# Performance work log

Hardware: AMD Instinct MI355X
Metric: run time of the kernel (lower is better)

## Reference

```python
import jax, jax.numpy as jnp
import numpy as np
from jax import lax

EPS = 1e-05


def rmsnorm_axis1(x, w, eps=EPS):
    # RMS over channel axis (axis=1), scale by per-channel weight
    ms = jnp.mean(x * x, axis=1, keepdims=True)
    return x * lax.rsqrt(ms + eps) * w[None, :, None]


def dwconv1d(x, w, b, dilation):
    # x: [B, C, L]; w: [C, 1, K] depthwise (feature_group_count=C)
    pad = (w.shape[-1] - 1) // 2 * dilation
    y = lax.conv_general_dilated(
        x, w, window_strides=(1,), padding=[(pad, pad)],
        rhs_dilation=(dilation,), dimension_numbers=('NCH', 'OIH', 'NCH'),
        feature_group_count=x.shape[1])
    return y + b[None, :, None]


def setup_inputs() -> dict:
    key = jax.random.key(0)
    ks = jax.random.split(key, 12)
    B, C, L, K = 16, 512, 2048, 3
    s = 1.0 / np.sqrt(C)
    return {
        'number_log': jax.random.normal(ks[0], (B,), jnp.float32),
        'x': jax.random.normal(ks[1], (B, C, L), jnp.float32),
        'pre_w': jnp.ones((C,), jnp.float32),
        'conv_w': jax.random.normal(ks[2], (C, 1, K), jnp.float32) * 0.3,
        'conv_b': jnp.zeros((C,), jnp.float32),
        'conv1_w': jax.random.normal(ks[3], (C, 1, K), jnp.float32) * 0.3,
        'conv1_b': jnp.zeros((C,), jnp.float32),
        'conv2_w': jax.random.normal(ks[4], (C, 1, K), jnp.float32) * 0.3,
        'conv2_b': jnp.zeros((C,), jnp.float32),
        'gate_w': jax.random.normal(ks[5], (C, C), jnp.float32) * s,
        'gate_b': jnp.zeros((C,), jnp.float32),
        'post_w': jnp.ones((C,), jnp.float32),
        'logits_w': jax.random.normal(ks[6], (1, C, 1), jnp.float32) * s,
    }


def reference(number_log, x, pre_w, conv_w, conv_b, conv1_w, conv1_b,
              conv2_w, conv2_b, gate_w, gate_b, post_w, logits_w):
    # pre_norm over channel axis
    x_norm = rmsnorm_axis1(x, pre_w)
    # three dilated depthwise conv branches, summed
    x_d = (dwconv1d(x_norm, conv_w, conv_b, 1)
           + dwconv1d(x_norm, conv1_w, conv1_b, 2)
           + dwconv1d(x_norm, conv2_w, conv2_b, 4))
    # gate: Linear over channel dim of transposed input, SiLU
    gate = jax.nn.silu(jnp.einsum('bcl,dc->bdl', x_norm, gate_w)
                       + gate_b[None, :, None])
    x_d = rmsnorm_axis1(x_d * gate, post_w)
    # logits: 1x1 conv C->1, no bias
    out = jnp.einsum('bcl,oc->bol', x + x_d, logits_w[:, :, 0])
    return out
```

## Files before the change

### kernel.cpp

```cpp
#include <hip/hip_runtime.h>
#include <hip/hip_bf16.h>

#define BB 16
#define CC 512
#define LL 2048

typedef float f32x4 __attribute__((ext_vector_type(4)));
typedef short s16x8 __attribute__((ext_vector_type(8)));

static __device__ __forceinline__ float bf2f(unsigned short u) {
    union { unsigned int i; float f; } v; v.i = ((unsigned int)u) << 16; return v.f;
}
static __device__ __forceinline__ unsigned short f2bf(float f) {
    union { float fv; unsigned int i; } v; v.fv = f;
    unsigned int x = v.i;
    return (unsigned short)((x + 0x7FFFu + ((x >> 16) & 1u)) >> 16);
}

__global__ void k0_cast(const float* __restrict__ gw, unsigned short* __restrict__ gwb) {
    int i = blockIdx.x * 256 + threadIdx.x;
    if (i < CC * CC) gwb[i] = f2bf(gw[i]);
}

#define K1_ST 520
__global__ __launch_bounds__(256) void k1_rms_t(
    const float* __restrict__ x, const float* __restrict__ pre_w,
    unsigned short* __restrict__ xnt, float* __restrict__ invr) {
    __shared__ unsigned short tile[32 * K1_ST];
    __shared__ float red[32 * 33];
    __shared__ float pwS[CC];
    __shared__ float ivS[32];
    const int tid = threadIdx.x;
    const int b  = blockIdx.x >> 6;
    const int lt = blockIdx.x & 63;
    const int l0 = lt * 32;
    const float* xb = x + (size_t)(b * CC) * LL + l0;

    for (int i = tid; i < CC; i += 256) pwS[i] = pre_w[i];

    const int lq = tid & 7;
    const int cr = tid >> 3;
    f32x4 ssq = {0.f, 0.f, 0.f, 0.f};
    #pragma unroll
    for (int p = 0; p < 16; ++p) {
        int c = p * 32 + cr;
        f32x4 v = *(const f32x4*)(xb + (size_t)c * LL + lq * 4);
        #pragma unroll
        for (int r = 0; r < 4; ++r) {
            ssq[r] += v[r] * v[r];
            tile[(lq * 4 + r) * K1_ST + c] = f2bf(v[r]);
        }
    }
    #pragma unroll
    for (int r = 0; r < 4; ++r) red[(lq * 4 + r) * 33 + cr] = ssq[r];
    __syncthreads();
    if (tid < 32) {
        float s = 0.f;
        #pragma unroll
        for (int g = 0; g < 32; ++g) s += red[tid * 33 + g];
        float iv = rsqrtf(s * (1.0f / CC) + 1e-5f);
        ivS[tid] = iv;
        invr[b * LL + l0 + tid] = iv;
    }
    __syncthreads();
    unsigned short* xo = xnt + ((size_t)b * LL + l0) * CC;
    #pragma unroll
    for (int p = 0; p < 8; ++p) {
        int g = p * 256 + tid;
        int l = g >> 6, c8 = (g & 63) * 8;
        s16x8 t = *(const s16x8*)&tile[l * K1_ST + c8];
        f32x4 w0 = *(const f32x4*)&pwS[c8];
        f32x4 w1 = *(const f32x4*)&pwS[c8 + 4];
        float iv = ivS[l];
        s16x8 o;
        #pragma unroll
        for (int r = 0; r < 4; ++r) {
            o[r]     = (short)f2bf(bf2f((unsigned short)t[r])     * iv * w0[r]);
            o[r + 4] = (short)f2bf(bf2f((unsigned short)t[r + 4]) * iv * w1[r]);
        }
        *(s16x8*)(xo + (size_t)l * CC + c8) = o;
    }
}

__global__ __launch_bounds__(512, 4) void k2_gemm(
    const unsigned short* __restrict__ gwb,
    const unsigned short* __restrict__ xnt,
    const float* __restrict__ gate_b,
    unsigned short* __restrict__ gate) {
    __shared__ unsigned short As[3][128 * 32];
    __shared__ unsigned short Bs[3][256 * 32];
    const int tid = threadIdx.x;
    const int w = tid >> 6, lane = tid & 63;
    const int lo = lane & 15, hi = lane >> 4;
    const int wm = w >> 2, wn = w & 3;
    const int nt = blockIdx.x, mt = blockIdx.y, b = blockIdx.z;
    const int m0 = mt * 128, n0 = nt * 256;
    const unsigned short* Ab = gwb;
    const unsigned short* Bb = xnt + (size_t)b * LL * CC;

    #define STG(kt_, buf_)                                                            \
        {                                                                             \
            {                                                                         \
                int row_ = tid >> 2, gin_ = tid & 3;                                  \
                int ks_ = (kt_) * 32 + ((gin_ ^ ((row_ >> 1) & 3)) * 8);              \
                __builtin_amdgcn_global_load_lds(                                     \
                    (const __attribute__((address_space(1))) void*)(Ab + (size_t)(m0 + row_) * CC + ks_), \
                    (__attribute__((address_space(3))) void*)(&As[buf_][tid * 8]),    \
                    16, 0, 0);                                                        \
            }                                                                         \
            _Pragma("unroll")                                                         \
            for (int s_ = 0; s_ < 2; ++s_) {                                          \
                int g_ = tid + s_ * 512;                                              \
                int row_ = g_ >> 2, gin_ = g_ & 3;                                    \
                int ks_ = (kt_) * 32 + ((gin_ ^ ((row_ >> 1) & 3)) * 8);              \
                __builtin_amdgcn_global_load_lds(                                     \
                    (const __attribute__((address_space(1))) void*)(Bb + (size_t)(n0 + row_) * CC + ks_), \
                    (__attribute__((address_space(3))) void*)(&Bs[buf_][g_ * 8]),     \
                    16, 0, 0);                                                        \
            }                                                                         \
        }

    f32x4 acc[4][4] = {};
    const int fsw = (lo >> 1) & 3;

    STG(0, 0);
    STG(1, 1);
    #pragma unroll
    for (int kt = 0; kt < 16; ++kt) {
        const int buf = kt % 3;
        if (kt < 14) {
            STG(kt + 2, (kt + 2) % 3);
            asm volatile("s_waitcnt vmcnt(6)" ::: "memory");
        } else if (kt == 14) {
            asm volatile("s_waitcnt vmcnt(3)" ::: "memory");
        } else {
            asm volatile("s_waitcnt vmcnt(0)" ::: "memory");
        }
        __builtin_amdgcn_s_barrier();
        s16x8 af[4], bfr[4];
        #pragma unroll
        for (int mi = 0; mi < 4; ++mi)
            af[mi] = *(const s16x8*)&As[buf][(wm * 64 + mi * 16 + lo) * 32 + ((hi ^ fsw) * 8)];
        #pragma unroll
        for (int ni = 0; ni < 4; ++ni)
            bfr[ni] = *(const s16x8*)&Bs[buf][(wn * 64 + ni * 16 + lo) * 32 + ((hi ^ fsw) * 8)];
        __builtin_amdgcn_s_setprio(1);
        #pragma unroll
        for (int mi = 0; mi < 4; ++mi)
            #pragma unroll
            for (int ni = 0; ni < 4; ++ni)
                acc[mi][ni] = __builtin_amdgcn_mfma_f32_16x16x32_bf16(
                    af[mi], bfr[ni], acc[mi][ni], 0, 0, 0);
        __builtin_amdgcn_s_setprio(0);
        asm volatile("" ::: "memory");
        __builtin_amdgcn_s_barrier();
    }
    #undef STG

    #pragma unroll
    for (int mi = 0; mi < 4; ++mi) {
        #pragma unroll
        for (int ni = 0; ni < 4; ++ni) {
            int n = n0 + wn * 64 + ni * 16 + lo;
            int d0 = m0 + wm * 64 + mi * 16 + hi * 4;
            #pragma unroll
            for (int r = 0; r < 4; ++r) {
                int d = d0 + r;
                float z = acc[mi][ni][r] + gate_b[d];
                float s = z / (1.0f + __expf(-z));
                gate[((size_t)(b * CC + d)) * LL + n] = f2bf(s);
            }
        }
    }
}

__global__ __launch_bounds__(256) void k3a(
    const float* __restrict__ x, const float* __restrict__ invr,
    const unsigned short* __restrict__ gate,
    const float* __restrict__ cw0, const float* __restrict__ cb0,
    const float* __restrict__ cw1, const float* __restrict__ cb1,
    const float* __restrict__ cw2, const float* __restrict__ cb2,
    const float* __restrict__ pre_w, const float* __restrict__ post_w,
    const float* __restrict__ lw, float* __restrict__ part) {
    __shared__ float tapS[64][8];
    __shared__ float biasS[64], preS[64], lwS[64], pwlwS[64];
    __shared__ float ivs[136];
    __shared__ float red[8][128][3];
    const int tid = threadIdx.x;
    const int lt = blockIdx.x;
    const int cc = blockIdx.y;
    const int b  = blockIdx.z;
    const int l0 = lt * 128;
    const int c0 = cc * 64;

    if (tid < 64) {
        int c = c0 + tid;
        float w10 = cw0[c*3], w11 = cw0[c*3+1], w12 = cw0[c*3+2];
        float w20 = cw1[c*3], w21 = cw1[c*3+1], w22 = cw1[c*3+2];
        float w40 = cw2[c*3], w41 = cw2[c*3+1], w42 = cw2[c*3+2];
        tapS[tid][0] = w40; tapS[tid][1] = w20; tapS[tid][2] = w10;
        tapS[tid][3] = w11 + w21 + w41;
        tapS[tid][4] = w12; tapS[tid][5] = w22; tapS[tid][6] = w42;
        biasS[tid] = cb0[c] + cb1[c] + cb2[c];
        preS[tid]  = pre_w[c];
        float lwc = lw[c];
        lwS[tid] = lwc;
        pwlwS[tid] = post_w[c] * lwc;
    }
    if (tid < 136) {
        int lg = l0 - 4 + tid;
        ivs[tid] = (lg >= 0 && lg < LL) ? invr[b * LL + lg] : 0.f;
    }
    __syncthreads();

    const int li = tid & 31, ci = tid >> 5;
    const int lq = l0 + li * 4;
    float iv[12];
    #pragma unroll
    for (int j = 0; j < 12; ++j) iv[j] = ivs[li * 4 + j];

    const int ia = (lq - 4 < 0) ? 0 : lq - 4;
    const int ic = (lq + 4 > LL - 4) ? LL - 4 : lq + 4;

    float ass[4] = {}, adp[4] = {}, adx[4] = {};
    const float* xbase = x + ((size_t)(b * CC + c0)) * LL;
    const unsigned short* gbase = gate + ((size_t)(b * CC + c0)) * LL;

    #pragma unroll
    for (int j = 0; j < 8; ++j) {
        const int cl = ci * 8 + j;
        const float* xr = xbase + (size_t)cl * LL;
        f32x4 xa = *(const f32x4*)(xr + ia);
        f32x4 xm = *(const f32x4*)(xr + lq);
        f32x4 xc = *(const f32x4*)(xr + ic);
        uint2 gu = *(const uint2*)(gbase + (size_t)cl * LL + lq);
        float g[4];
        g[0] = bf2f((unsigned short)(gu.x & 0xffff));
        g[1] = bf2f((unsigned short)(gu.x >> 16));
        g[2] = bf2f((unsigned short)(gu.y & 0xffff));
        g[3] = bf2f((unsigned short)(gu.y >> 16));
        float z[12];
        #pragma unroll
        for (int r = 0; r < 4; ++r) {
            z[r]     = xa[r] * iv[r];
            z[r + 4] = xm[r] * iv[r + 4];
            z[r + 8] = xc[r] * iv[r + 8];
        }
        const float t0 = tapS[cl][0], t1 = tapS[cl][1], t2 = tapS[cl][2],
                    t3 = tapS[cl][3], t4 = tapS[cl][4], t5 = tapS[cl][5],
                    t6 = tapS[cl][6];
        const float pre = preS[cl], bias = biasS[cl], pwlw = pwlwS[cl], lwc = lwS[cl];
        #pragma unroll
        for (int k = 0; k < 4; ++k) {
            float s = t0 * z[k] + t1 * z[k + 2] + t2 * z[k + 3] + t3 * z[k + 4]
                    + t4 * z[k + 5] + t5 * z[k + 6] + t6 * z[k + 8];
            float p = (pre * s + bias) * g[k];
            ass[k] += p * p;
            adp[k] += p * pwlw;
            adx[k] += xm[k] * lwc;
        }
    }
    #pragma unroll
    for (int k = 0; k < 4; ++k) {
        red[ci][li * 4 + k][0] = ass[k];
        red[ci][li * 4 + k][1] = adp[k];
        red[ci][li * 4 + k][2] = adx[k];
    }
    __syncthreads();
    if (tid < 128) {
        float s0 = 0.f, s1 = 0.f, s2 = 0.f;
        #pragma unroll
        for (int g2 = 0; g2 < 8; ++g2) {
            s0 += red[g2][tid][0];
            s1 += red[g2][tid][1];
            s2 += red[g2][tid][2];
        }
        float* pp = part + (((size_t)(b * 8 + cc)) * LL + l0 + tid) * 3;
        pp[0] = s0; pp[1] = s1; pp[2] = s2;
    }
}

__global__ __launch_bounds__(256) void k3b(
    const float* __restrict__ part, float* __restrict__ out) {
    int gl = blockIdx.x * 256 + threadIdx.x;
    int b = gl >> 11, l = gl & 2047;
    float s0 = 0.f, s1 = 0.f, s2 = 0.f;
    #pragma unroll
    for (int cc2 = 0; cc2 < 8; ++cc2) {
        const float* pp = part + (((size_t)(b * 8 + cc2)) * LL + l) * 3;
        s0 += pp[0]; s1 += pp[1]; s2 += pp[2];
    }
    out[gl] = s2 + rsqrtf(s0 * (1.0f / CC) + 1e-5f) * s1;
}

extern "C" void kernel_launch(void* const* d_in, const int* in_sizes, int n_in,
                              void* d_out, int out_size, void* d_ws, size_t ws_size,
                              hipStream_t stream) {
    const float* x      = (const float*)d_in[1];
    const float* pre_w  = (const float*)d_in[2];
    const float* cw0    = (const float*)d_in[3];
    const float* cb0    = (const float*)d_in[4];
    const float* cw1    = (const float*)d_in[5];
    const float* cb1    = (const float*)d_in[6];
    const float* cw2    = (const float*)d_in[7];
    const float* cb2    = (const float*)d_in[8];
    const float* gw     = (const float*)d_in[9];
    const float* gb     = (const float*)d_in[10];
    const float* post_w = (const float*)d_in[11];
    const float* lw     = (const float*)d_in[12];
    float* out = (float*)d_out;

    char* ws = (char*)d_ws;
    unsigned short* gwb  = (unsigned short*)(ws);
    unsigned short* xnt  = (unsigned short*)(ws + 524288);
    float*          invr = (float*)(ws + 524288 + 33554432);
    unsigned short* gate = (unsigned short*)(ws + 524288 + 33554432 + 131072);
    float*          part = (float*)(ws + 524288);

    hipLaunchKernelGGL(k0_cast,  dim3((CC * CC + 255) / 256), dim3(256), 0, stream, gw, gwb);
    hipLaunchKernelGGL(k1_rms_t, dim3(BB * (LL / 32)),        dim3(256), 0, stream, x, pre_w, xnt, invr);
    hipLaunchKernelGGL(k2_gemm,  dim3(LL / 256, CC / 128, BB), dim3(512), 0, stream, gwb, xnt, gb, gate);
    hipLaunchKernelGGL(k3a,      dim3(LL / 128, CC / 64, BB), dim3(256), 0, stream,
                       x, invr, gate, cw0, cb0, cw1, cb1, cw2, cb2, pre_w, post_w, lw, part);
    hipLaunchKernelGGL(k3b,      dim3(BB * LL / 256),         dim3(256), 0, stream, part, out);
}
```

Baseline: 78.60 us.

## Drop LDS staging in gate GEMM, load MFMA fragments directly from global

The gate GEMM no longer stages A and B tiles through a triple-buffered LDS pipeline with barriers. Each wave instead loads its MFMA fragments straight from global memory (relying on L1/L2) and computes a 64x64 tile, with blocks shrunk to 256 threads and a 64-row M tile. This removes the barrier and LDS traffic overhead but loses cross-wave reuse, since the A tile is loaded by all four waves. It also drops explicit prefetching, which exposes global-load latency per k-step.

```diff
diff --git a/kernel.cpp b/kernel.cpp
--- a/kernel.cpp
+++ b/kernel.cpp
@@ -82,87 +82,45 @@
     }
 }
 
-__global__ __launch_bounds__(512, 4) void k2_gemm(
+__global__ __launch_bounds__(256, 3) void k2_gemm(
     const unsigned short* __restrict__ gwb,
     const unsigned short* __restrict__ xnt,
     const float* __restrict__ gate_b,
     unsigned short* __restrict__ gate) {
-    __shared__ unsigned short As[3][128 * 32];
-    __shared__ unsigned short Bs[3][256 * 32];
     const int tid = threadIdx.x;
     const int w = tid >> 6, lane = tid & 63;
     const int lo = lane & 15, hi = lane >> 4;
-    const int wm = w >> 2, wn = w & 3;
     const int nt = blockIdx.x, mt = blockIdx.y, b = blockIdx.z;
-    const int m0 = mt * 128, n0 = nt * 256;
-    const unsigned short* Ab = gwb;
-    const unsigned short* Bb = xnt + (size_t)b * LL * CC;
-
-    #define STG(kt_, buf_)                                                            \
-        {                                                                             \
-            {                                                                         \
-                int row_ = tid >> 2, gin_ = tid & 3;                                  \
-                int ks_ = (kt_) * 32 + ((gin_ ^ ((row_ >> 1) & 3)) * 8);              \
-                __builtin_amdgcn_global_load_lds(                                     \
-                    (const __attribute__((address_space(1))) void*)(Ab + (size_t)(m0 + row_) * CC + ks_), \
-                    (__attribute__((address_space(3))) void*)(&As[buf_][tid * 8]),    \
-                    16, 0, 0);                                                        \
-            }                                                                         \
-            _Pragma("unroll")                                                         \
-            for (int s_ = 0; s_ < 2; ++s_) {                                          \
-                int g_ = tid + s_ * 512;                                              \
-                int row_ = g_ >> 2, gin_ = g_ & 3;                                    \
-                int ks_ = (kt_) * 32 + ((gin_ ^ ((row_ >> 1) & 3)) * 8);              \
-                __builtin_amdgcn_global_load_lds(                                     \
-                    (const __attribute__((address_space(1))) void*)(Bb + (size_t)(n0 + row_) * CC + ks_), \
-                    (__attribute__((address_space(3))) void*)(&Bs[buf_][g_ * 8]),     \
-                    16, 0, 0);                                                        \
-            }                                                                         \
-        }
+    const int m0 = mt * 64;
+    const int n0 = nt * 256 + w * 64;
+
+    const unsigned short* Ap = gwb + (size_t)(m0 + lo) * CC + hi * 8;
+    const unsigned short* Bp = xnt + (size_t)b * LL * CC + (size_t)(n0 + lo) * CC + hi * 8;
 
     f32x4 acc[4][4] = {};
-    const int fsw = (lo >> 1) & 3;
-
-    STG(0, 0);
-    STG(1, 1);
-    #pragma unroll
-    for (int kt = 0; kt < 16; ++kt) {
-        const int buf = kt % 3;
-        if (kt < 14) {
-            STG(kt + 2, (kt + 2) % 3);
-            asm volatile("s_waitcnt vmcnt(6)" ::: "memory");
-        } else if (kt == 14) {
-            asm volatile("s_waitcnt vmcnt(3)" ::: "memory");
-        } else {
-            asm volatile("s_waitcnt vmcnt(0)" ::: "memory");
-        }
-        __builtin_amdgcn_s_barrier();
+    #pragma unroll
+    for (int ks = 0; ks < 16; ++ks) {
         s16x8 af[4], bfr[4];
         #pragma unroll
         for (int mi = 0; mi < 4; ++mi)
-            af[mi] = *(const s16x8*)&As[buf][(wm * 64 + mi * 16 + lo) * 32 + ((hi ^ fsw) * 8)];
+            af[mi] = *(const s16x8*)(Ap + (size_t)mi * 16 * CC + ks * 32);
         #pragma unroll
         for (int ni = 0; ni < 4; ++ni)
-            bfr[ni] = *(const s16x8*)&Bs[buf][(wn * 64 + ni * 16 + lo) * 32 + ((hi ^ fsw) * 8)];
-        __builtin_amdgcn_s_setprio(1);
+            bfr[ni] = *(const s16x8*)(Bp + (size_t)ni * 16 * CC + ks * 32);
         #pragma unroll
         for (int mi = 0; mi < 4; ++mi)
             #pragma unroll
             for (int ni = 0; ni < 4; ++ni)
                 acc[mi][ni] = __builtin_amdgcn_mfma_f32_16x16x32_bf16(
                     af[mi], bfr[ni], acc[mi][ni], 0, 0, 0);
-        __builtin_amdgcn_s_setprio(0);
-        asm volatile("" ::: "memory");
-        __builtin_amdgcn_s_barrier();
-    }
-    #undef STG
+    }
 
     #pragma unroll
     for (int mi = 0; mi < 4; ++mi) {
         #pragma unroll
         for (int ni = 0; ni < 4; ++ni) {
-            int n = n0 + wn * 64 + ni * 16 + lo;
-            int d0 = m0 + wm * 64 + mi * 16 + hi * 4;
+            int n = n0 + ni * 16 + lo;
+            int d0 = m0 + mi * 16 + hi * 4;
             #pragma unroll
             for (int r = 0; r < 4; ++r) {
                 int d = d0 + r;
@@ -319,7 +277,7 @@
 
     hipLaunchKernelGGL(k0_cast,  dim3((CC * CC + 255) / 256), dim3(256), 0, stream, gw, gwb);
     hipLaunchKernelGGL(k1_rms_t, dim3(BB * (LL / 32)),        dim3(256), 0, stream, x, pre_w, xnt, invr);
-    hipLaunchKernelGGL(k2_gemm,  dim3(LL / 256, CC / 128, BB), dim3(512), 0, stream, gwb, xnt, gb, gate);
+    hipLaunchKernelGGL(k2_gemm,  dim3(LL / 256, CC / 64, BB), dim3(256), 0, stream, gwb, xnt, gb, gate);
     hipLaunchKernelGGL(k3a,      dim3(LL / 128, CC / 64, BB), dim3(256), 0, stream,
                        x, invr, gate, cw0, cb0, cw1, cb1, cw2, cb2, pre_w, post_w, lw, part);
     hipLaunchKernelGGL(k3b,      dim3(BB * LL / 256),         dim3(256), 0, stream, part, out);
```

Result: slower. 117.7 us (+49.7%).
